# Kernel tuning notes

Measured on AMD Instinct MI355X. Metric: run time of the kernel, lower is better.

Reference implementation:

```python
import jax, jax.numpy as jnp
import numpy as np

NUM_HEADS = 8  # init num_heads


def setup_inputs() -> dict:
    key = jax.random.key(0)
    ks = jax.random.split(key, 8)
    B, N, C, G = 2, 256 * 256, 256, 512  # N hardcoded by original reshape(256*256)
    xq = jax.random.normal(ks[0], (B, N, C), jnp.float32)
    xk = jax.random.normal(ks[1], (B, N, C), jnp.float32)
    xv = jax.random.normal(ks[2], (B, N, C), jnp.float32)
    w_scale = C ** -0.5
    Wq = jax.random.normal(ks[3], (C, C), jnp.float32) * w_scale
    bq = jax.random.normal(ks[4], (C,), jnp.float32) * 0.02
    Wp = jax.random.normal(ks[5], (C, C), jnp.float32) * w_scale
    bp = jax.random.normal(ks[6], (C,), jnp.float32) * 0.02
    # Voronoi cell labels 1..G, each cell exactly N//G tokens, randomly scattered
    # over the 256x256 grid (irregular gather/scatter access, all cells < 1500 tokens).
    labels = jnp.repeat(jnp.arange(1, G + 1, dtype=jnp.int32), N // G)
    Voronoi = jnp.stack([
        jax.random.permutation(jax.random.fold_in(ks[7], b), labels) for b in range(B)
    ]).reshape(B, 256, 256)
    return {"xq": xq, "xk": xk, "xv": xv, "Wq": Wq, "bq": bq,
            "Wp": Wp, "bp": bp, "Voronoi": Voronoi, "num_groups": G}


def reference(xq, xk, xv, Wq, bq, Wp, bp, Voronoi, num_groups):
    B, N, C = xq.shape
    H = NUM_HEADS
    hd = C // H
    scale = hd ** -0.5  # qk_scale default: head_dim ** -0.5
    # NOTE: the original forward projects q, k AND v with self.q (shared weights/bias).
    # This (likely a bug upstream) is preserved faithfully here.
    q = (xq @ Wq.T + bq).reshape(B, N, H, hd)
    k = (xk @ Wq.T + bq).reshape(B, N, H, hd)
    v = (xv @ Wq.T + bq).reshape(B, N, H, hd)
    labels = Voronoi.reshape(B, N)
    order = jnp.argsort(labels, axis=1)   # [B, N] sort tokens by Voronoi cell id
    inv = jnp.argsort(order, axis=1)      # inverse permutation for scatter-back
    S = N // num_groups                   # tokens per cell (static)

    def gather(t):  # [B, N, H, hd] -> [B, G, S, H, hd] grouped by cell
        return jnp.take_along_axis(t, order[:, :, None, None], axis=1).reshape(B, num_groups, S, H, hd)

    qg = gather(q) * scale
    kg = gather(k)
    vg = gather(v)
    attn = jnp.einsum('bgshd,bgthd->bghst', qg, kg)   # per-cell scores [B,G,H,S,S]
    p = jax.nn.softmax(attn, axis=-1)                 # attn_drop=0 (eval)
    og = jnp.einsum('bghst,bgthd->bgshd', p, vg).reshape(B, N, H, hd)
    out = jnp.take_along_axis(og, inv[:, :, None, None], axis=1).reshape(B, N, C)
    return out @ Wp.T + bp                            # proj_drop=0 (eval)
```

## Files before the change

### kernel.cpp

```cpp
#include <hip/hip_runtime.h>
#include <hip/hip_bf16.h>

#define B_    2
#define NTOK  65536
#define C_    256
#define H_    8
#define HD_   32
#define G_    512
#define S_    128
#define BN    (B_*NTOK)
#define M3    (3*BN)

typedef __attribute__((ext_vector_type(8))) short short8;
typedef __attribute__((ext_vector_type(4))) float f32x4;

__device__ __forceinline__ ushort f2bf(float f) {
  __bf16 h = (__bf16)f;
  return __builtin_bit_cast(unsigned short, h);
}
__device__ __forceinline__ unsigned pk2(float lo, float hi) {
  return (unsigned)f2bf(lo) | ((unsigned)f2bf(hi) << 16);
}

__device__ __forceinline__ void gl16(const void* g, void* l) {
  __builtin_amdgcn_global_load_lds(
      (const __attribute__((address_space(1))) unsigned int*)g,
      (__attribute__((address_space(3))) unsigned int*)l, 16, 0, 0);
}

#define SW4(c, r) ((((c) ^ (r) ^ ((r) >> 2))) & 3)

__global__ __launch_bounds__(256) void k_prep(const float* __restrict__ Wq,
                                              const float* __restrict__ Wp,
                                              ushort* __restrict__ Wq_img,
                                              ushort* __restrict__ Wp_img) {
  int gid = blockIdx.x * 256 + threadIdx.x;
  int w = gid >> 13, rem = gid & 8191;
  int ks = rem >> 11, rem2 = rem & 2047;
  int r = rem2 >> 3, c = rem2 & 7;
  const float* W = w ? Wp : Wq;
  ushort* img = w ? Wp_img : Wq_img;
  const float4* s = reinterpret_cast<const float4*>(W + (size_t)r * 256 + ks * 64 + c * 8);
  float4 a = s[0], b = s[1];
  uint4 o;
  o.x = pk2(a.x, a.y); o.y = pk2(a.z, a.w);
  o.z = pk2(b.x, b.y); o.w = pk2(b.z, b.w);
  *reinterpret_cast<uint4*>(img + ks * 16384 + r * 64 + ((c ^ (r & 7)) << 3)) = o;
}

__global__ __launch_bounds__(256) void k_group(const int* __restrict__ vor,
                                               int* __restrict__ grp,
                                               int* __restrict__ cnt) {
  int idx = blockIdx.x * 256 + threadIdx.x;
  int b = idx >> 16;
  int n = idx & (NTOK - 1);
  int g = vor[idx] - 1;
  int pos = atomicAdd(&cnt[(b << 9) + g], 1);
  grp[((b << 9) + g) * S_ + pos] = n;
}

__global__ __launch_bounds__(512, 4) void k_proj_qkv(
    const float* __restrict__ xq, const float* __restrict__ xk,
    const float* __restrict__ xv, const ushort* __restrict__ Wq_img,
    const float* __restrict__ bq, ushort* __restrict__ qkv) {
  __shared__ ushort As[128 * 64];
  __shared__ ushort Bs[2][256 * 64];
  int mt = blockIdx.x;
  int t = mt >> 10;
  const float* A = (t == 0) ? xq : (t == 1) ? xk : xv;
  size_t abase = (size_t)(mt & 1023) * 128 * 256;
  int row0 = mt * 128;

  int tid = threadIdx.x, lane = tid & 63, wave = tid >> 6;
  int l15 = lane & 15, hi = lane >> 4;
  int wr = (wave >> 2) * 64, wc = (wave & 3) * 64;
  int sr = tid >> 2, sq = tid & 3;

  const float* aptr = A + abase + (size_t)sr * 256 + sq * 16;
  int boff = wave * 4096 + lane * 16;

  f32x4 acc[4][4] = {};
  float4 ar[2][4];
  {
    const float4* p = reinterpret_cast<const float4*>(aptr);
#pragma unroll
    for (int j = 0; j < 4; ++j) ar[0][j] = p[j];
  }
#pragma unroll
  for (int j = 0; j < 4; ++j)
    gl16((const char*)Wq_img + boff + j * 1024, (char*)Bs[0] + boff + j * 1024);

#pragma unroll
  for (int ks = 0; ks < 4; ++ks) {
    uint4 w0, w1;
    w0.x = pk2(ar[ks & 1][0].x, ar[ks & 1][0].y); w0.y = pk2(ar[ks & 1][0].z, ar[ks & 1][0].w);
    w0.z = pk2(ar[ks & 1][1].x, ar[ks & 1][1].y); w0.w = pk2(ar[ks & 1][1].z, ar[ks & 1][1].w);
    w1.x = pk2(ar[ks & 1][2].x, ar[ks & 1][2].y); w1.y = pk2(ar[ks & 1][2].z, ar[ks & 1][2].w);
    w1.z = pk2(ar[ks & 1][3].x, ar[ks & 1][3].y); w1.w = pk2(ar[ks & 1][3].z, ar[ks & 1][3].w);
    *reinterpret_cast<uint4*>(&As[sr * 64 + (((sq * 2) ^ (sr & 7)) << 3)]) = w0;
    *reinterpret_cast<uint4*>(&As[sr * 64 + (((sq * 2 + 1) ^ (sr & 7)) << 3)]) = w1;
    if (ks < 3) {
      const float4* p = reinterpret_cast<const float4*>(aptr + (ks + 1) * 64);
#pragma unroll
      for (int j = 0; j < 4; ++j) ar[(ks + 1) & 1][j] = p[j];
#pragma unroll
      for (int j = 0; j < 4; ++j)
        gl16((const char*)Wq_img + (ks + 1) * 32768 + boff + j * 1024,
             (char*)Bs[(ks + 1) & 1] + boff + j * 1024);
      asm volatile("s_waitcnt vmcnt(8)" ::: "memory");
    } else {
      asm volatile("s_waitcnt vmcnt(0)" ::: "memory");
    }
    asm volatile("s_waitcnt lgkmcnt(0)" ::: "memory");
    __builtin_amdgcn_s_barrier();
    const ushort* Bcur = Bs[ks & 1];
#pragma unroll
    for (int kk = 0; kk < 2; ++kk) {
      int ck = kk * 4 + hi;
      short8 af[4], bfr[4];
#pragma unroll
      for (int m = 0; m < 4; ++m) {
        int r = wr + m * 16 + l15;
        af[m] = *reinterpret_cast<const short8*>(&As[r * 64 + ((ck ^ (r & 7)) << 3)]);
      }
#pragma unroll
      for (int n = 0; n < 4; ++n) {
        int r = wc + n * 16 + l15;
        bfr[n] = *reinterpret_cast<const short8*>(&Bcur[r * 64 + ((ck ^ (r & 7)) << 3)]);
      }
#pragma unroll
      for (int m = 0; m < 4; ++m)
#pragma unroll
        for (int n = 0; n < 4; ++n)
          acc[m][n] = __builtin_amdgcn_mfma_f32_16x16x32_bf16(af[m], bfr[n], acc[m][n], 0, 0, 0);
    }
    asm volatile("s_waitcnt lgkmcnt(0)" ::: "memory");
    __builtin_amdgcn_s_barrier();
  }

  ushort* Ot = (ushort*)Bs;
#pragma unroll
  for (int n = 0; n < 4; ++n) {
    int col = wc + n * 16 + l15;
    float bv = bq[col];
    int c = col >> 3, ci = col & 7;
#pragma unroll
    for (int m = 0; m < 4; ++m) {
      int r0 = wr + m * 16 + hi * 4;
#pragma unroll
      for (int j = 0; j < 4; ++j) {
        int r = r0 + j;
        int slot = c ^ (((r >> 2) & 3) << 1);
        Ot[r * 256 + slot * 8 + ci] = f2bf(acc[m][n][j] + bv);
      }
    }
  }
  __syncthreads();
  {
    size_t gbase = (size_t)row0 * 256;
#pragma unroll
    for (int s = 0; s < 8; ++s) {
      int off = s * 4096 + tid * 8;
      int r = off >> 8, cc = (off >> 3) & 31;
      int slot = cc ^ (((r >> 2) & 3) << 1);
      *reinterpret_cast<uint4*>(qkv + gbase + off) =
          *reinterpret_cast<const uint4*>(Ot + r * 256 + slot * 8);
    }
  }
}

__global__ __launch_bounds__(256) void k_attn(const ushort* __restrict__ qkv,
                                              const int* __restrict__ grp,
                                              ushort* __restrict__ attn_out) {
  __shared__ int toks[128];
  __shared__ ushort PsB[128 * 128];
  __shared__ ushort Vt[32 * 128];
  ushort* Qs = PsB;
  ushort* Ks = PsB + 4096;
  ushort* Ps = PsB;

  int bid = blockIdx.x;
  int h = bid & 7, g = (bid >> 3) & (G_ - 1), b = bid >> 12;
  int tid = threadIdx.x, lane = tid & 63, wave = tid >> 6;
  int l15 = lane & 15, hi = lane >> 4;

  if (tid < 128) toks[tid] = grp[((b << 9) + g) * S_ + tid];
  __syncthreads();

  {
    int r = tid >> 1;
    int cp = (tid & 1) * 2;
    int tok = toks[r];
    size_t rowq = (size_t)(b * NTOK + tok) * 256 + h * 32;
    const uint4* q4 = reinterpret_cast<const uint4*>(qkv + rowq + cp * 8);
    const uint4* k4 = reinterpret_cast<const uint4*>(qkv + (size_t)BN * 256 + rowq + cp * 8);
    const uint4* v4 = reinterpret_cast<const uint4*>(qkv + (size_t)2 * BN * 256 + rowq + cp * 8);
    uint4 qa = q4[0], qb = q4[1];
    uint4 ka = k4[0], kb = k4[1];
    uint4 va = v4[0], vb = v4[1];
    *reinterpret_cast<uint4*>(&Qs[r * 32 + SW4(cp, r) * 8]) = qa;
    *reinterpret_cast<uint4*>(&Qs[r * 32 + SW4(cp + 1, r) * 8]) = qb;
    *reinterpret_cast<uint4*>(&Ks[r * 32 + SW4(cp, r) * 8]) = ka;
    *reinterpret_cast<uint4*>(&Ks[r * 32 + SW4(cp + 1, r) * 8]) = kb;
    int chunk_t = r >> 3, tl = r & 7;
    const ushort* pva = reinterpret_cast<const ushort*>(&va);
    const ushort* pvb = reinterpret_cast<const ushort*>(&vb);
#pragma unroll
    for (int e = 0; e < 8; ++e) {
      int ch = cp * 8 + e;
      Vt[ch * 128 + ((chunk_t ^ ((ch & 7) << 1)) << 3) + tl] = pva[e];
      int ch2 = ch + 8;
      Vt[ch2 * 128 + ((chunk_t ^ ((ch2 & 7) << 1)) << 3) + tl] = pvb[e];
    }
  }
  __syncthreads();

  f32x4 sacc[2][8] = {};
  {
    short8 aq[2], bk[8];
#pragma unroll
    for (int m = 0; m < 2; ++m) {
      int r = wave * 32 + m * 16 + l15;
      aq[m] = *reinterpret_cast<const short8*>(&Qs[r * 32 + SW4(hi, r) * 8]);
    }
#pragma unroll
    for (int n = 0; n < 8; ++n) {
      int r = n * 16 + l15;
      bk[n] = *reinterpret_cast<const short8*>(&Ks[r * 32 + SW4(hi, r) * 8]);
    }
#pragma unroll
    for (int m = 0; m < 2; ++m)
#pragma unroll
      for (int n = 0; n < 8; ++n)
        sacc[m][n] = __builtin_amdgcn_mfma_f32_16x16x32_bf16(aq[m], bk[n], sacc[m][n], 0, 0, 0);
  }
  __syncthreads();

  const float cexp = 0.17677669529663687f * 1.4426950408889634f;
#pragma unroll
  for (int m = 0; m < 2; ++m) {
#pragma unroll
    for (int j = 0; j < 4; ++j) {
      float mx = -1e30f;
#pragma unroll
      for (int n = 0; n < 8; ++n) mx = fmaxf(mx, sacc[m][n][j]);
#pragma unroll
      for (int d = 1; d < 16; d <<= 1) mx = fmaxf(mx, __shfl_xor(mx, d));
      float pv[8], sum = 0.f;
#pragma unroll
      for (int n = 0; n < 8; ++n) { pv[n] = exp2f((sacc[m][n][j] - mx) * cexp); sum += pv[n]; }
#pragma unroll
      for (int d = 1; d < 16; d <<= 1) sum += __shfl_xor(sum, d);
      float inv = 1.0f / sum;
      int row = wave * 32 + m * 16 + hi * 4 + j;
#pragma unroll
      for (int n = 0; n < 8; ++n) {
        int col = n * 16 + l15;
        int chunk = col >> 3;
        Ps[row * 128 + ((chunk ^ (row & 7)) << 3) + (col & 7)] = f2bf(pv[n] * inv);
      }
    }
  }
  __syncthreads();

  f32x4 oacc[2][2] = {};
#pragma unroll
  for (int kk = 0; kk < 4; ++kk) {
    int k0 = kk * 32 + hi * 8;
    int chunk = k0 >> 3;
    short8 pa[2], bv[2];
#pragma unroll
    for (int m = 0; m < 2; ++m) {
      int r = wave * 32 + m * 16 + l15;
      pa[m] = *reinterpret_cast<const short8*>(&Ps[r * 128 + ((chunk ^ (r & 7)) << 3)]);
    }
#pragma unroll
    for (int n = 0; n < 2; ++n) {
      int ch = n * 16 + l15;
      bv[n] = *reinterpret_cast<const short8*>(&Vt[ch * 128 + ((chunk ^ ((ch & 7) << 1)) << 3)]);
    }
#pragma unroll
    for (int m = 0; m < 2; ++m)
#pragma unroll
      for (int n = 0; n < 2; ++n)
        oacc[m][n] = __builtin_amdgcn_mfma_f32_16x16x32_bf16(pa[m], bv[n], oacc[m][n], 0, 0, 0);
  }

  __syncthreads();
  ushort* Ot = Ps;
#pragma unroll
  for (int m = 0; m < 2; ++m) {
    int rb = wave * 32 + m * 16 + hi * 4;
#pragma unroll
    for (int j = 0; j < 4; ++j)
#pragma unroll
      for (int n = 0; n < 2; ++n)
        Ot[(rb + j) * 32 + n * 16 + l15] = f2bf(oacc[m][n][j]);
  }
  __syncthreads();
  {
    int tr = tid >> 1, part = tid & 1;
    int tok = toks[tr];
    size_t base = ((size_t)(b * NTOK + tok)) * 256 + h * 32 + part * 16;
    const uint4* src = reinterpret_cast<const uint4*>(Ot + tr * 32 + part * 16);
    uint4 v0 = src[0], v1 = src[1];
    *reinterpret_cast<uint4*>(attn_out + base) = v0;
    *reinterpret_cast<uint4*>(attn_out + base + 8) = v1;
  }
}

__global__ __launch_bounds__(512, 4) void k_proj_out(
    const ushort* __restrict__ Abf, const ushort* __restrict__ Wp_img,
    const float* __restrict__ bp, float* __restrict__ out) {
  __shared__ ushort As[128 * 64];
  __shared__ ushort Bs[2][256 * 64];
  int mt = blockIdx.x;
  int row0 = mt * 128;

  int tid = threadIdx.x, lane = tid & 63, wave = tid >> 6;
  int l15 = lane & 15, hi = lane >> 4;
  int wr = (wave >> 2) * 64, wc = (wave & 3) * 64;
  int sr = tid >> 2, sq = tid & 3;

  const ushort* aptr = Abf + (size_t)(row0 + sr) * 256 + sq * 16;
  int boff = wave * 4096 + lane * 16;

  f32x4 acc[4][4] = {};
  uint4 ar[2][2];
  {
    const uint4* p = reinterpret_cast<const uint4*>(aptr);
    ar[0][0] = p[0]; ar[0][1] = p[1];
  }
#pragma unroll
  for (int j = 0; j < 4; ++j)
    gl16((const char*)Wp_img + boff + j * 1024, (char*)Bs[0] + boff + j * 1024);

#pragma unroll
  for (int ks = 0; ks < 4; ++ks) {
    *reinterpret_cast<uint4*>(&As[sr * 64 + (((sq * 2) ^ (sr & 7)) << 3)]) = ar[ks & 1][0];
    *reinterpret_cast<uint4*>(&As[sr * 64 + (((sq * 2 + 1) ^ (sr & 7)) << 3)]) = ar[ks & 1][1];
    if (ks < 3) {
      const uint4* p = reinterpret_cast<const uint4*>(aptr + (ks + 1) * 64);
      ar[(ks + 1) & 1][0] = p[0]; ar[(ks + 1) & 1][1] = p[1];
#pragma unroll
      for (int j = 0; j < 4; ++j)
        gl16((const char*)Wp_img + (ks + 1) * 32768 + boff + j * 1024,
             (char*)Bs[(ks + 1) & 1] + boff + j * 1024);
      asm volatile("s_waitcnt vmcnt(6)" ::: "memory");
    } else {
      asm volatile("s_waitcnt vmcnt(0)" ::: "memory");
    }
    asm volatile("s_waitcnt lgkmcnt(0)" ::: "memory");
    __builtin_amdgcn_s_barrier();
    const ushort* Bcur = Bs[ks & 1];
#pragma unroll
    for (int kk = 0; kk < 2; ++kk) {
      int ck = kk * 4 + hi;
      short8 af[4], bfr[4];
#pragma unroll
      for (int m = 0; m < 4; ++m) {
        int r = wr + m * 16 + l15;
        af[m] = *reinterpret_cast<const short8*>(&As[r * 64 + ((ck ^ (r & 7)) << 3)]);
      }
#pragma unroll
      for (int n = 0; n < 4; ++n) {
        int r = wc + n * 16 + l15;
        bfr[n] = *reinterpret_cast<const short8*>(&Bcur[r * 64 + ((ck ^ (r & 7)) << 3)]);
      }
#pragma unroll
      for (int m = 0; m < 4; ++m)
#pragma unroll
        for (int n = 0; n < 4; ++n)
          acc[m][n] = __builtin_amdgcn_mfma_f32_16x16x32_bf16(af[m], bfr[n], acc[m][n], 0, 0, 0);
    }
    asm volatile("s_waitcnt lgkmcnt(0)" ::: "memory");
    __builtin_amdgcn_s_barrier();
  }

  float* Of = (float*)Bs;
#pragma unroll
  for (int hf = 0; hf < 2; ++hf) {
    if (hf) __syncthreads();
    if ((wave >> 2) == hf) {
#pragma unroll
      for (int n = 0; n < 4; ++n) {
        int col = wc + n * 16 + l15;
        float bv = bp[col];
        int c = col >> 2, ci = col & 3;
#pragma unroll
        for (int m = 0; m < 4; ++m) {
          int lr = m * 16 + hi * 4;
#pragma unroll
          for (int j = 0; j < 4; ++j) {
            int r = lr + j;
            int slot = c ^ (((r >> 2) & 3) << 2);
            Of[r * 256 + slot * 4 + ci] = acc[m][n][j] + bv;
          }
        }
      }
    }
    __syncthreads();
    size_t gbase = (size_t)(row0 + hf * 64) * 256;
#pragma unroll
    for (int s = 0; s < 8; ++s) {
      int off = s * 2048 + tid * 4;
      int r = off >> 8, cc = (off >> 2) & 63;
      int slot = cc ^ (((r >> 2) & 3) << 2);
      *reinterpret_cast<float4*>(out + gbase + off) =
          *reinterpret_cast<const float4*>(Of + r * 256 + slot * 4);
    }
  }
}

extern "C" void kernel_launch(void* const* d_in, const int* in_sizes, int n_in,
                              void* d_out, int out_size, void* d_ws, size_t ws_size,
                              hipStream_t stream) {
  const float* xq = (const float*)d_in[0];
  const float* xk = (const float*)d_in[1];
  const float* xv = (const float*)d_in[2];
  const float* Wq = (const float*)d_in[3];
  const float* bq = (const float*)d_in[4];
  const float* Wp = (const float*)d_in[5];
  const float* bp = (const float*)d_in[6];
  const int*   vor = (const int*)d_in[7];

  char* ws = (char*)d_ws;
  ushort* qkv    = (ushort*)ws;
  ushort* attn   = (ushort*)(ws + (size_t)201326592);
  int*    grp    = (int*)(ws + (size_t)268435456);
  int*    cnt    = (int*)(ws + (size_t)268959744);
  ushort* Wq_img = (ushort*)(ws + (size_t)268963840);
  ushort* Wp_img = (ushort*)(ws + (size_t)269094912);

  hipMemsetAsync(cnt, 0, B_ * G_ * sizeof(int), stream);
  k_prep<<<dim3(64), dim3(256), 0, stream>>>(Wq, Wp, Wq_img, Wp_img);
  k_group<<<dim3(BN / 256), dim3(256), 0, stream>>>(vor, grp, cnt);
  k_proj_qkv<<<dim3(M3 / 128), dim3(512), 0, stream>>>(xq, xk, xv, Wq_img, bq, qkv);
  k_attn<<<dim3(B_ * G_ * H_), dim3(256), 0, stream>>>(qkv, grp, attn);
  k_proj_out<<<dim3(BN / 128), dim3(512), 0, stream>>>(attn, Wp_img, bp, (float*)d_out);
}
```

Measured before the change: 318.1 us.

## Split QKV projection into 128x128 tiles with K=32 double-buffered pipeline

The QKV projection kernel now uses 256-thread blocks that each compute a 128x128 output tile, so twice as many blocks are launched. The K loop runs in 8 steps of 32 instead of 4 steps of 64. Both the A and the weight tiles are double-buffered, so the next step's global loads overlap the current MFMA step. The weight image layout and its swizzle are rebuilt to match the K=32 tiling. The aim is more blocks and more overlap per CU, at the cost of reading and converting the fp32 activations twice (once per column half) and running more barriers.

Measured after the change: 342.4 us. +7.6%, slower.

```diff
diff --git a/kernel.cpp b/kernel.cpp
--- a/kernel.cpp
+++ b/kernel.cpp
@@ -29,6 +29,7 @@
 }
 
 #define SW4(c, r) ((((c) ^ (r) ^ ((r) >> 2))) & 3)
+#define SWK32(c, r) ((((c) ^ ((r) >> 1))) & 3)
 
 __global__ __launch_bounds__(256) void k_prep(const float* __restrict__ Wq,
                                               const float* __restrict__ Wp,
@@ -36,16 +37,24 @@
                                               ushort* __restrict__ Wp_img) {
   int gid = blockIdx.x * 256 + threadIdx.x;
   int w = gid >> 13, rem = gid & 8191;
-  int ks = rem >> 11, rem2 = rem & 2047;
-  int r = rem2 >> 3, c = rem2 & 7;
-  const float* W = w ? Wp : Wq;
-  ushort* img = w ? Wp_img : Wq_img;
-  const float4* s = reinterpret_cast<const float4*>(W + (size_t)r * 256 + ks * 64 + c * 8);
-  float4 a = s[0], b = s[1];
-  uint4 o;
-  o.x = pk2(a.x, a.y); o.y = pk2(a.z, a.w);
-  o.z = pk2(b.x, b.y); o.w = pk2(b.z, b.w);
-  *reinterpret_cast<uint4*>(img + ks * 16384 + r * 64 + ((c ^ (r & 7)) << 3)) = o;
+  if (w == 0) {
+    int ks = rem >> 10, r = (rem >> 2) & 255, c = rem & 3;
+    const float4* s = reinterpret_cast<const float4*>(Wq + (size_t)r * 256 + ks * 32 + c * 8);
+    float4 a = s[0], b = s[1];
+    uint4 o;
+    o.x = pk2(a.x, a.y); o.y = pk2(a.z, a.w);
+    o.z = pk2(b.x, b.y); o.w = pk2(b.z, b.w);
+    *reinterpret_cast<uint4*>(Wq_img + ks * 8192 + r * 32 + (SWK32(c, r) << 3)) = o;
+  } else {
+    int ks = rem >> 11, rem2 = rem & 2047;
+    int r = rem2 >> 3, c = rem2 & 7;
+    const float4* s = reinterpret_cast<const float4*>(Wp + (size_t)r * 256 + ks * 64 + c * 8);
+    float4 a = s[0], b = s[1];
+    uint4 o;
+    o.x = pk2(a.x, a.y); o.y = pk2(a.z, a.w);
+    o.z = pk2(b.x, b.y); o.w = pk2(b.z, b.w);
+    *reinterpret_cast<uint4*>(Wp_img + ks * 16384 + r * 64 + ((c ^ (r & 7)) << 3)) = o;
+  }
 }
 
 __global__ __launch_bounds__(256) void k_group(const int* __restrict__ vor,
@@ -59,112 +68,133 @@
   grp[((b << 9) + g) * S_ + pos] = n;
 }
 
-__global__ __launch_bounds__(512, 4) void k_proj_qkv(
+__global__ __launch_bounds__(256, 4) void k_proj_qkv(
     const float* __restrict__ xq, const float* __restrict__ xk,
     const float* __restrict__ xv, const ushort* __restrict__ Wq_img,
     const float* __restrict__ bq, ushort* __restrict__ qkv) {
-  __shared__ ushort As[128 * 64];
-  __shared__ ushort Bs[2][256 * 64];
-  int mt = blockIdx.x;
+  __shared__ ushort lds[24576];
+  ushort* AsB[2] = { lds, lds + 4096 };
+  ushort* BsB[2] = { lds + 8192, lds + 16384 };
+  BsB[0] = lds + 8192; BsB[1] = lds + 12288;
+
+  int bid = blockIdx.x;
+  int mt = bid >> 1, nt = bid & 1;
   int t = mt >> 10;
   const float* A = (t == 0) ? xq : (t == 1) ? xk : xv;
   size_t abase = (size_t)(mt & 1023) * 128 * 256;
-  int row0 = mt * 128;
+  int row0 = mt * 128, col0 = nt * 128;
 
   int tid = threadIdx.x, lane = tid & 63, wave = tid >> 6;
   int l15 = lane & 15, hi = lane >> 4;
-  int wr = (wave >> 2) * 64, wc = (wave & 3) * 64;
-  int sr = tid >> 2, sq = tid & 3;
-
-  const float* aptr = A + abase + (size_t)sr * 256 + sq * 16;
-  int boff = wave * 4096 + lane * 16;
+  int wr = (wave >> 1) * 64, wc = (wave & 1) * 64;
+  int sr = tid >> 1, sc2 = (tid & 1) * 2;
+
+  const float* aptr = A + abase + (size_t)sr * 256 + sc2 * 8;
+  const char* bimg = (const char*)Wq_img + nt * 8192;
+  int boff = wave * 2048 + lane * 16;
 
   f32x4 acc[4][4] = {};
-  float4 ar[2][4];
+  float4 a[2][4];
+
   {
     const float4* p = reinterpret_cast<const float4*>(aptr);
 #pragma unroll
-    for (int j = 0; j < 4; ++j) ar[0][j] = p[j];
-  }
-#pragma unroll
-  for (int j = 0; j < 4; ++j)
-    gl16((const char*)Wq_img + boff + j * 1024, (char*)Bs[0] + boff + j * 1024);
-
-#pragma unroll
-  for (int ks = 0; ks < 4; ++ks) {
+    for (int j = 0; j < 4; ++j) a[0][j] = p[j];
+  }
+  gl16(bimg + boff, (char*)BsB[0] + boff);
+  gl16(bimg + boff + 1024, (char*)BsB[0] + boff + 1024);
+  {
+    const float4* p = reinterpret_cast<const float4*>(aptr + 32);
+#pragma unroll
+    for (int j = 0; j < 4; ++j) a[1][j] = p[j];
+  }
+  {
     uint4 w0, w1;
-    w0.x = pk2(ar[ks & 1][0].x, ar[ks & 1][0].y); w0.y = pk2(ar[ks & 1][0].z, ar[ks & 1][0].w);
-    w0.z = pk2(ar[ks & 1][1].x, ar[ks & 1][1].y); w0.w = pk2(ar[ks & 1][1].z, ar[ks & 1][1].w);
-    w1.x = pk2(ar[ks & 1][2].x, ar[ks & 1][2].y); w1.y = pk2(ar[ks & 1][2].z, ar[ks & 1][2].w);
-    w1.z = pk2(ar[ks & 1][3].x, ar[ks & 1][3].y); w1.w = pk2(ar[ks & 1][3].z, ar[ks & 1][3].w);
-    *reinterpret_cast<uint4*>(&As[sr * 64 + (((sq * 2) ^ (sr & 7)) << 3)]) = w0;
-    *reinterpret_cast<uint4*>(&As[sr * 64 + (((sq * 2 + 1) ^ (sr & 7)) << 3)]) = w1;
-    if (ks < 3) {
-      const float4* p = reinterpret_cast<const float4*>(aptr + (ks + 1) * 64);
-#pragma unroll
-      for (int j = 0; j < 4; ++j) ar[(ks + 1) & 1][j] = p[j];
-#pragma unroll
-      for (int j = 0; j < 4; ++j)
-        gl16((const char*)Wq_img + (ks + 1) * 32768 + boff + j * 1024,
-             (char*)Bs[(ks + 1) & 1] + boff + j * 1024);
-      asm volatile("s_waitcnt vmcnt(8)" ::: "memory");
+    w0.x = pk2(a[0][0].x, a[0][0].y); w0.y = pk2(a[0][0].z, a[0][0].w);
+    w0.z = pk2(a[0][1].x, a[0][1].y); w0.w = pk2(a[0][1].z, a[0][1].w);
+    w1.x = pk2(a[0][2].x, a[0][2].y); w1.y = pk2(a[0][2].z, a[0][2].w);
+    w1.z = pk2(a[0][3].x, a[0][3].y); w1.w = pk2(a[0][3].z, a[0][3].w);
+    *reinterpret_cast<uint4*>(&AsB[0][sr * 32 + (SWK32(sc2, sr) << 3)]) = w0;
+    *reinterpret_cast<uint4*>(&AsB[0][sr * 32 + (SWK32(sc2 + 1, sr) << 3)]) = w1;
+  }
+  asm volatile("s_waitcnt vmcnt(4)" ::: "memory");
+  asm volatile("s_waitcnt lgkmcnt(0)" ::: "memory");
+  __builtin_amdgcn_s_barrier();
+
+#pragma unroll
+  for (int ks = 0; ks < 8; ++ks) {
+    const int cur = ks & 1, alt = cur ^ 1;
+    if (ks < 7) {
+      gl16(bimg + (ks + 1) * 16384 + boff, (char*)BsB[alt] + boff);
+      gl16(bimg + (ks + 1) * 16384 + boff + 1024, (char*)BsB[alt] + boff + 1024);
+      uint4 w0, w1;
+      w0.x = pk2(a[alt][0].x, a[alt][0].y); w0.y = pk2(a[alt][0].z, a[alt][0].w);
+      w0.z = pk2(a[alt][1].x, a[alt][1].y); w0.w = pk2(a[alt][1].z, a[alt][1].w);
+      w1.x = pk2(a[alt][2].x, a[alt][2].y); w1.y = pk2(a[alt][2].z, a[alt][2].w);
+      w1.z = pk2(a[alt][3].x, a[alt][3].y); w1.w = pk2(a[alt][3].z, a[alt][3].w);
+      *reinterpret_cast<uint4*>(&AsB[alt][sr * 32 + (SWK32(sc2, sr) << 3)]) = w0;
+      *reinterpret_cast<uint4*>(&AsB[alt][sr * 32 + (SWK32(sc2 + 1, sr) << 3)]) = w1;
+    }
+    if (ks < 6) {
+      const float4* p = reinterpret_cast<const float4*>(aptr + (ks + 2) * 32);
+#pragma unroll
+      for (int j = 0; j < 4; ++j) a[cur][j] = p[j];
+    }
+    {
+      const ushort* Ac = AsB[cur];
+      const ushort* Bc = BsB[cur];
+      short8 af[4], bf[4];
+#pragma unroll
+      for (int m = 0; m < 4; ++m) {
+        int r = wr + m * 16 + l15;
+        af[m] = *reinterpret_cast<const short8*>(&Ac[r * 32 + (SWK32(hi, r) << 3)]);
+      }
+#pragma unroll
+      for (int n = 0; n < 4; ++n) {
+        int r = wc + n * 16 + l15;
+        bf[n] = *reinterpret_cast<const short8*>(&Bc[r * 32 + (SWK32(hi, r) << 3)]);
+      }
+#pragma unroll
+      for (int m = 0; m < 4; ++m)
+#pragma unroll
+        for (int n = 0; n < 4; ++n)
+          acc[m][n] = __builtin_amdgcn_mfma_f32_16x16x32_bf16(af[m], bf[n], acc[m][n], 0, 0, 0);
+    }
+    if (ks < 6) {
+      asm volatile("s_waitcnt vmcnt(4)" ::: "memory");
     } else {
       asm volatile("s_waitcnt vmcnt(0)" ::: "memory");
     }
     asm volatile("s_waitcnt lgkmcnt(0)" ::: "memory");
     __builtin_amdgcn_s_barrier();
-    const ushort* Bcur = Bs[ks & 1];
-#pragma unroll
-    for (int kk = 0; kk < 2; ++kk) {
-      int ck = kk * 4 + hi;
-      short8 af[4], bfr[4];
-#pragma unroll
-      for (int m = 0; m < 4; ++m) {
-        int r = wr + m * 16 + l15;
-        af[m] = *reinterpret_cast<const short8*>(&As[r * 64 + ((ck ^ (r & 7)) << 3)]);
-      }
-#pragma unroll
-      for (int n = 0; n < 4; ++n) {
-        int r = wc + n * 16 + l15;
-        bfr[n] = *reinterpret_cast<const short8*>(&Bcur[r * 64 + ((ck ^ (r & 7)) << 3)]);
-      }
-#pragma unroll
-      for (int m = 0; m < 4; ++m)
-#pragma unroll
-        for (int n = 0; n < 4; ++n)
-          acc[m][n] = __builtin_amdgcn_mfma_f32_16x16x32_bf16(af[m], bfr[n], acc[m][n], 0, 0, 0);
-    }
-    asm volatile("s_waitcnt lgkmcnt(0)" ::: "memory");
-    __builtin_amdgcn_s_barrier();
-  }
-
-  ushort* Ot = (ushort*)Bs;
+  }
+
+  ushort* Ot = lds;
 #pragma unroll
   for (int n = 0; n < 4; ++n) {
-    int col = wc + n * 16 + l15;
-    float bv = bq[col];
-    int c = col >> 3, ci = col & 7;
+    int lc = wc + n * 16 + l15;
+    float bv = bq[col0 + lc];
+    int c = lc >> 3, ci = lc & 7;
 #pragma unroll
     for (int m = 0; m < 4; ++m) {
       int r0 = wr + m * 16 + hi * 4;
 #pragma unroll
       for (int j = 0; j < 4; ++j) {
         int r = r0 + j;
-        int slot = c ^ (((r >> 2) & 3) << 1);
-        Ot[r * 256 + slot * 8 + ci] = f2bf(acc[m][n][j] + bv);
-      }
-    }
-  }
-  __syncthreads();
-  {
-    size_t gbase = (size_t)row0 * 256;
+        int slot = (c ^ ((r >> 2) & 3)) & 15;
+        Ot[r * 128 + slot * 8 + ci] = f2bf(acc[m][n][j] + bv);
+      }
+    }
+  }
+  __syncthreads();
+  {
 #pragma unroll
     for (int s = 0; s < 8; ++s) {
-      int off = s * 4096 + tid * 8;
-      int r = off >> 8, cc = (off >> 3) & 31;
-      int slot = cc ^ (((r >> 2) & 3) << 1);
-      *reinterpret_cast<uint4*>(qkv + gbase + off) =
-          *reinterpret_cast<const uint4*>(Ot + r * 256 + slot * 8);
+      int i = s * 2048 + tid * 8;
+      int r = i >> 7, c = (tid & 15);
+      int slot = (c ^ ((r >> 2) & 3)) & 15;
+      *reinterpret_cast<uint4*>(qkv + (size_t)(row0 + r) * 256 + col0 + c * 8) =
+          *reinterpret_cast<const uint4*>(Ot + r * 128 + slot * 8);
     }
   }
 }
@@ -435,7 +465,7 @@
   hipMemsetAsync(cnt, 0, B_ * G_ * sizeof(int), stream);
   k_prep<<<dim3(64), dim3(256), 0, stream>>>(Wq, Wp, Wq_img, Wp_img);
   k_group<<<dim3(BN / 256), dim3(256), 0, stream>>>(vor, grp, cnt);
-  k_proj_qkv<<<dim3(M3 / 128), dim3(512), 0, stream>>>(xq, xk, xv, Wq_img, bq, qkv);
+  k_proj_qkv<<<dim3((M3 / 128) * 2), dim3(256), 0, stream>>>(xq, xk, xv, Wq_img, bq, qkv);
   k_attn<<<dim3(B_ * G_ * H_), dim3(256), 0, stream>>>(qkv, grp, attn);
   k_proj_out<<<dim3(BN / 128), dim3(512), 0, stream>>>(attn, Wp_img, bp, (float*)d_out);
 }
```

## Fuse attention and output projection into one per-cell kernel

Applied to the files above, without the earlier changes.

Merges the per-(cell,head) attention kernel and the output projection GEMM into a single kernel in which each block handles one Voronoi cell and loops over all 8 heads. Each head's output is accumulated straight into the projection result through a per-head Wp slice staged in LDS, and the final fp32 result is scattered to token rows. This removes the bf16 attention intermediate write/read and one kernel launch. In exchange there are far fewer blocks (1024 instead of 8192), a serial head loop with many barriers, larger LDS use per block, and scattered row writes to the output.

After: 341.7 us. 1.07x slower.

```diff
diff --git a/kernel.cpp b/kernel.cpp
--- a/kernel.cpp
+++ b/kernel.cpp
@@ -29,6 +29,7 @@
 }
 
 #define SW4(c, r) ((((c) ^ (r) ^ ((r) >> 2))) & 3)
+#define SWK32(c, r) ((((c) ^ ((r) >> 1))) & 3)
 
 __global__ __launch_bounds__(256) void k_prep(const float* __restrict__ Wq,
                                               const float* __restrict__ Wp,
@@ -36,16 +37,24 @@
                                               ushort* __restrict__ Wp_img) {
   int gid = blockIdx.x * 256 + threadIdx.x;
   int w = gid >> 13, rem = gid & 8191;
-  int ks = rem >> 11, rem2 = rem & 2047;
-  int r = rem2 >> 3, c = rem2 & 7;
-  const float* W = w ? Wp : Wq;
-  ushort* img = w ? Wp_img : Wq_img;
-  const float4* s = reinterpret_cast<const float4*>(W + (size_t)r * 256 + ks * 64 + c * 8);
-  float4 a = s[0], b = s[1];
-  uint4 o;
-  o.x = pk2(a.x, a.y); o.y = pk2(a.z, a.w);
-  o.z = pk2(b.x, b.y); o.w = pk2(b.z, b.w);
-  *reinterpret_cast<uint4*>(img + ks * 16384 + r * 64 + ((c ^ (r & 7)) << 3)) = o;
+  if (w == 0) {
+    int ks = rem >> 11, rem2 = rem & 2047;
+    int r = rem2 >> 3, c = rem2 & 7;
+    const float4* s = reinterpret_cast<const float4*>(Wq + (size_t)r * 256 + ks * 64 + c * 8);
+    float4 a = s[0], b = s[1];
+    uint4 o;
+    o.x = pk2(a.x, a.y); o.y = pk2(a.z, a.w);
+    o.z = pk2(b.x, b.y); o.w = pk2(b.z, b.w);
+    *reinterpret_cast<uint4*>(Wq_img + ks * 16384 + r * 64 + ((c ^ (r & 7)) << 3)) = o;
+  } else {
+    int h = rem >> 10, r = (rem >> 2) & 255, c = rem & 3;
+    const float4* s = reinterpret_cast<const float4*>(Wp + (size_t)r * 256 + h * 32 + c * 8);
+    float4 a = s[0], b = s[1];
+    uint4 o;
+    o.x = pk2(a.x, a.y); o.y = pk2(a.z, a.w);
+    o.z = pk2(b.x, b.y); o.w = pk2(b.z, b.w);
+    *reinterpret_cast<uint4*>(Wp_img + h * 8192 + r * 32 + (SWK32(c, r) << 3)) = o;
+  }
 }
 
 __global__ __launch_bounds__(256) void k_group(const int* __restrict__ vor,
@@ -169,90 +178,90 @@
   }
 }
 
-__global__ __launch_bounds__(256) void k_attn(const ushort* __restrict__ qkv,
-                                              const int* __restrict__ grp,
-                                              ushort* __restrict__ attn_out) {
+__global__ __launch_bounds__(512) void k_attn_proj(
+    const ushort* __restrict__ qkv, const int* __restrict__ grp,
+    const ushort* __restrict__ Wp_img, const float* __restrict__ bp,
+    float* __restrict__ out) {
   __shared__ int toks[128];
   __shared__ ushort PsB[128 * 128];
   __shared__ ushort Vt[32 * 128];
+  __shared__ ushort Oh[128 * 32];
+  __shared__ ushort WpS[256 * 32];
   ushort* Qs = PsB;
   ushort* Ks = PsB + 4096;
   ushort* Ps = PsB;
 
   int bid = blockIdx.x;
-  int h = bid & 7, g = (bid >> 3) & (G_ - 1), b = bid >> 12;
+  int g = bid & (G_ - 1), b = bid >> 9;
   int tid = threadIdx.x, lane = tid & 63, wave = tid >> 6;
   int l15 = lane & 15, hi = lane >> 4;
+  int strip = wave * 16;
+  int mg = wave >> 1, ng = wave & 1;
 
   if (tid < 128) toks[tid] = grp[((b << 9) + g) * S_ + tid];
   __syncthreads();
 
-  {
-    int r = tid >> 1;
-    int cp = (tid & 1) * 2;
-    int tok = toks[r];
-    size_t rowq = (size_t)(b * NTOK + tok) * 256 + h * 32;
-    const uint4* q4 = reinterpret_cast<const uint4*>(qkv + rowq + cp * 8);
-    const uint4* k4 = reinterpret_cast<const uint4*>(qkv + (size_t)BN * 256 + rowq + cp * 8);
-    const uint4* v4 = reinterpret_cast<const uint4*>(qkv + (size_t)2 * BN * 256 + rowq + cp * 8);
-    uint4 qa = q4[0], qb = q4[1];
-    uint4 ka = k4[0], kb = k4[1];
-    uint4 va = v4[0], vb = v4[1];
-    *reinterpret_cast<uint4*>(&Qs[r * 32 + SW4(cp, r) * 8]) = qa;
-    *reinterpret_cast<uint4*>(&Qs[r * 32 + SW4(cp + 1, r) * 8]) = qb;
-    *reinterpret_cast<uint4*>(&Ks[r * 32 + SW4(cp, r) * 8]) = ka;
-    *reinterpret_cast<uint4*>(&Ks[r * 32 + SW4(cp + 1, r) * 8]) = kb;
-    int chunk_t = r >> 3, tl = r & 7;
-    const ushort* pva = reinterpret_cast<const ushort*>(&va);
-    const ushort* pvb = reinterpret_cast<const ushort*>(&vb);
-#pragma unroll
-    for (int e = 0; e < 8; ++e) {
-      int ch = cp * 8 + e;
-      Vt[ch * 128 + ((chunk_t ^ ((ch & 7) << 1)) << 3) + tl] = pva[e];
-      int ch2 = ch + 8;
-      Vt[ch2 * 128 + ((chunk_t ^ ((ch2 & 7) << 1)) << 3) + tl] = pvb[e];
-    }
-  }
-  __syncthreads();
-
-  f32x4 sacc[2][8] = {};
-  {
-    short8 aq[2], bk[8];
-#pragma unroll
-    for (int m = 0; m < 2; ++m) {
-      int r = wave * 32 + m * 16 + l15;
-      aq[m] = *reinterpret_cast<const short8*>(&Qs[r * 32 + SW4(hi, r) * 8]);
-    }
-#pragma unroll
-    for (int n = 0; n < 8; ++n) {
-      int r = n * 16 + l15;
-      bk[n] = *reinterpret_cast<const short8*>(&Ks[r * 32 + SW4(hi, r) * 8]);
-    }
-#pragma unroll
-    for (int m = 0; m < 2; ++m)
+  int wpoff = wave * 1024 + lane * 16;
+  gl16((const char*)Wp_img + wpoff, (char*)WpS + wpoff);
+  gl16((const char*)Wp_img + 8192 + wpoff, (char*)WpS + wpoff + 8192);
+
+  f32x4 acc[2][8] = {};
+
+  int r_st = tid >> 2, cp = tid & 3;
+  int tok_st = toks[r_st];
+  size_t rowq = (size_t)(b * NTOK + tok_st) * 256;
+
+  for (int h = 0; h < 8; ++h) {
+    {
+      size_t base = rowq + h * 32 + cp * 8;
+      uint4 qa = *reinterpret_cast<const uint4*>(qkv + base);
+      uint4 ka = *reinterpret_cast<const uint4*>(qkv + (size_t)BN * 256 + base);
+      uint4 va = *reinterpret_cast<const uint4*>(qkv + (size_t)2 * BN * 256 + base);
+      *reinterpret_cast<uint4*>(&Qs[r_st * 32 + SW4(cp, r_st) * 8]) = qa;
+      *reinterpret_cast<uint4*>(&Ks[r_st * 32 + SW4(cp, r_st) * 8]) = ka;
+      int chunk_t = r_st >> 3, tl = r_st & 7;
+      const ushort* pv_ = reinterpret_cast<const ushort*>(&va);
+#pragma unroll
+      for (int e = 0; e < 8; ++e) {
+        int ch = cp * 8 + e;
+        Vt[ch * 128 + ((chunk_t ^ ((ch & 7) << 1)) << 3) + tl] = pv_[e];
+      }
+    }
+    asm volatile("s_waitcnt lgkmcnt(0)" ::: "memory");
+    __builtin_amdgcn_s_barrier();
+
+    f32x4 sacc[8] = {};
+    {
+      int ra = strip + l15;
+      short8 aq = *reinterpret_cast<const short8*>(&Qs[ra * 32 + SW4(hi, ra) * 8]);
+      short8 bk[8];
+#pragma unroll
+      for (int n = 0; n < 8; ++n) {
+        int r = n * 16 + l15;
+        bk[n] = *reinterpret_cast<const short8*>(&Ks[r * 32 + SW4(hi, r) * 8]);
+      }
 #pragma unroll
       for (int n = 0; n < 8; ++n)
-        sacc[m][n] = __builtin_amdgcn_mfma_f32_16x16x32_bf16(aq[m], bk[n], sacc[m][n], 0, 0, 0);
-  }
-  __syncthreads();
-
-  const float cexp = 0.17677669529663687f * 1.4426950408889634f;
-#pragma unroll
-  for (int m = 0; m < 2; ++m) {
+        sacc[n] = __builtin_amdgcn_mfma_f32_16x16x32_bf16(aq, bk[n], sacc[n], 0, 0, 0);
+    }
+    asm volatile("s_waitcnt lgkmcnt(0)" ::: "memory");
+    __builtin_amdgcn_s_barrier();
+
+    const float cexp = 0.17677669529663687f * 1.4426950408889634f;
 #pragma unroll
     for (int j = 0; j < 4; ++j) {
       float mx = -1e30f;
 #pragma unroll
-      for (int n = 0; n < 8; ++n) mx = fmaxf(mx, sacc[m][n][j]);
+      for (int n = 0; n < 8; ++n) mx = fmaxf(mx, sacc[n][j]);
 #pragma unroll
       for (int d = 1; d < 16; d <<= 1) mx = fmaxf(mx, __shfl_xor(mx, d));
       float pv[8], sum = 0.f;
 #pragma unroll
-      for (int n = 0; n < 8; ++n) { pv[n] = exp2f((sacc[m][n][j] - mx) * cexp); sum += pv[n]; }
+      for (int n = 0; n < 8; ++n) { pv[n] = exp2f((sacc[n][j] - mx) * cexp); sum += pv[n]; }
 #pragma unroll
       for (int d = 1; d < 16; d <<= 1) sum += __shfl_xor(sum, d);
       float inv = 1.0f / sum;
-      int row = wave * 32 + m * 16 + hi * 4 + j;
+      int row = strip + hi * 4 + j;
 #pragma unroll
       for (int n = 0; n < 8; ++n) {
         int col = n * 16 + l15;
@@ -260,154 +269,94 @@
         Ps[row * 128 + ((chunk ^ (row & 7)) << 3) + (col & 7)] = f2bf(pv[n] * inv);
       }
     }
-  }
-  __syncthreads();
-
-  f32x4 oacc[2][2] = {};
-#pragma unroll
-  for (int kk = 0; kk < 4; ++kk) {
-    int k0 = kk * 32 + hi * 8;
-    int chunk = k0 >> 3;
-    short8 pa[2], bv[2];
-#pragma unroll
-    for (int m = 0; m < 2; ++m) {
-      int r = wave * 32 + m * 16 + l15;
-      pa[m] = *reinterpret_cast<const short8*>(&Ps[r * 128 + ((chunk ^ (r & 7)) << 3)]);
+    asm volatile("s_waitcnt lgkmcnt(0)" ::: "memory");
+    __builtin_amdgcn_s_barrier();
+
+    f32x4 oacc[2] = {};
+#pragma unroll
+    for (int kk = 0; kk < 4; ++kk) {
+      int chunk = kk * 4 + hi;
+      int rp = strip + l15;
+      short8 pa = *reinterpret_cast<const short8*>(&Ps[rp * 128 + ((chunk ^ (rp & 7)) << 3)]);
+      short8 bv[2];
+#pragma unroll
+      for (int n = 0; n < 2; ++n) {
+        int ch = n * 16 + l15;
+        bv[n] = *reinterpret_cast<const short8*>(&Vt[ch * 128 + ((chunk ^ ((ch & 7) << 1)) << 3)]);
+      }
+#pragma unroll
+      for (int n = 0; n < 2; ++n)
+        oacc[n] = __builtin_amdgcn_mfma_f32_16x16x32_bf16(pa, bv[n], oacc[n], 0, 0, 0);
     }
 #pragma unroll
     for (int n = 0; n < 2; ++n) {
-      int ch = n * 16 + l15;
-      bv[n] = *reinterpret_cast<const short8*>(&Vt[ch * 128 + ((chunk ^ ((ch & 7) << 1)) << 3)]);
-    }
-#pragma unroll
-    for (int m = 0; m < 2; ++m)
-#pragma unroll
-      for (int n = 0; n < 2; ++n)
-        oacc[m][n] = __builtin_amdgcn_mfma_f32_16x16x32_bf16(pa[m], bv[n], oacc[m][n], 0, 0, 0);
-  }
-
-  __syncthreads();
-  ushort* Ot = Ps;
-#pragma unroll
-  for (int m = 0; m < 2; ++m) {
-    int rb = wave * 32 + m * 16 + hi * 4;
-#pragma unroll
-    for (int j = 0; j < 4; ++j)
-#pragma unroll
-      for (int n = 0; n < 2; ++n)
-        Ot[(rb + j) * 32 + n * 16 + l15] = f2bf(oacc[m][n][j]);
-  }
-  __syncthreads();
-  {
-    int tr = tid >> 1, part = tid & 1;
-    int tok = toks[tr];
-    size_t base = ((size_t)(b * NTOK + tok)) * 256 + h * 32 + part * 16;
-    const uint4* src = reinterpret_cast<const uint4*>(Ot + tr * 32 + part * 16);
-    uint4 v0 = src[0], v1 = src[1];
-    *reinterpret_cast<uint4*>(attn_out + base) = v0;
-    *reinterpret_cast<uint4*>(attn_out + base + 8) = v1;
-  }
-}
-
-__global__ __launch_bounds__(512, 4) void k_proj_out(
-    const ushort* __restrict__ Abf, const ushort* __restrict__ Wp_img,
-    const float* __restrict__ bp, float* __restrict__ out) {
-  __shared__ ushort As[128 * 64];
-  __shared__ ushort Bs[2][256 * 64];
-  int mt = blockIdx.x;
-  int row0 = mt * 128;
-
-  int tid = threadIdx.x, lane = tid & 63, wave = tid >> 6;
-  int l15 = lane & 15, hi = lane >> 4;
-  int wr = (wave >> 2) * 64, wc = (wave & 3) * 64;
-  int sr = tid >> 2, sq = tid & 3;
-
-  const ushort* aptr = Abf + (size_t)(row0 + sr) * 256 + sq * 16;
-  int boff = wave * 4096 + lane * 16;
-
-  f32x4 acc[4][4] = {};
-  uint4 ar[2][2];
-  {
-    const uint4* p = reinterpret_cast<const uint4*>(aptr);
-    ar[0][0] = p[0]; ar[0][1] = p[1];
-  }
-#pragma unroll
-  for (int j = 0; j < 4; ++j)
-    gl16((const char*)Wp_img + boff + j * 1024, (char*)Bs[0] + boff + j * 1024);
-
-#pragma unroll
-  for (int ks = 0; ks < 4; ++ks) {
-    *reinterpret_cast<uint4*>(&As[sr * 64 + (((sq * 2) ^ (sr & 7)) << 3)]) = ar[ks & 1][0];
-    *reinterpret_cast<uint4*>(&As[sr * 64 + (((sq * 2 + 1) ^ (sr & 7)) << 3)]) = ar[ks & 1][1];
-    if (ks < 3) {
-      const uint4* p = reinterpret_cast<const uint4*>(aptr + (ks + 1) * 64);
-      ar[(ks + 1) & 1][0] = p[0]; ar[(ks + 1) & 1][1] = p[1];
-#pragma unroll
-      for (int j = 0; j < 4; ++j)
-        gl16((const char*)Wp_img + (ks + 1) * 32768 + boff + j * 1024,
-             (char*)Bs[(ks + 1) & 1] + boff + j * 1024);
-      asm volatile("s_waitcnt vmcnt(6)" ::: "memory");
-    } else {
-      asm volatile("s_waitcnt vmcnt(0)" ::: "memory");
-    }
-    asm volatile("s_waitcnt lgkmcnt(0)" ::: "memory");
-    __builtin_amdgcn_s_barrier();
-    const ushort* Bcur = Bs[ks & 1];
-#pragma unroll
-    for (int kk = 0; kk < 2; ++kk) {
-      int ck = kk * 4 + hi;
-      short8 af[4], bfr[4];
-#pragma unroll
-      for (int m = 0; m < 4; ++m) {
-        int r = wr + m * 16 + l15;
-        af[m] = *reinterpret_cast<const short8*>(&As[r * 64 + ((ck ^ (r & 7)) << 3)]);
-      }
-#pragma unroll
-      for (int n = 0; n < 4; ++n) {
-        int r = wc + n * 16 + l15;
-        bfr[n] = *reinterpret_cast<const short8*>(&Bcur[r * 64 + ((ck ^ (r & 7)) << 3)]);
-      }
-#pragma unroll
-      for (int m = 0; m < 4; ++m)
-#pragma unroll
-        for (int n = 0; n < 4; ++n)
-          acc[m][n] = __builtin_amdgcn_mfma_f32_16x16x32_bf16(af[m], bfr[n], acc[m][n], 0, 0, 0);
-    }
-    asm volatile("s_waitcnt lgkmcnt(0)" ::: "memory");
-    __builtin_amdgcn_s_barrier();
-  }
-
-  float* Of = (float*)Bs;
-#pragma unroll
-  for (int hf = 0; hf < 2; ++hf) {
-    if (hf) __syncthreads();
-    if ((wave >> 2) == hf) {
-#pragma unroll
-      for (int n = 0; n < 4; ++n) {
-        int col = wc + n * 16 + l15;
+#pragma unroll
+      for (int j = 0; j < 4; ++j) {
+        int row = strip + hi * 4 + j;
+        int col = n * 16 + l15;
+        Oh[row * 32 + (SWK32(col >> 3, row) << 3) + (col & 7)] = f2bf(oacc[n][j]);
+      }
+    }
+    asm volatile("s_waitcnt vmcnt(0)" ::: "memory");
+    asm volatile("s_waitcnt lgkmcnt(0)" ::: "memory");
+    __builtin_amdgcn_s_barrier();
+
+    {
+      short8 af[2], bf[8];
+#pragma unroll
+      for (int m = 0; m < 2; ++m) {
+        int r = mg * 32 + m * 16 + l15;
+        af[m] = *reinterpret_cast<const short8*>(&Oh[r * 32 + (SWK32(hi, r) << 3)]);
+      }
+#pragma unroll
+      for (int n = 0; n < 8; ++n) {
+        int r = ng * 128 + n * 16 + l15;
+        bf[n] = *reinterpret_cast<const short8*>(&WpS[r * 32 + (SWK32(hi, r) << 3)]);
+      }
+#pragma unroll
+      for (int m = 0; m < 2; ++m)
+#pragma unroll
+        for (int n = 0; n < 8; ++n)
+          acc[m][n] = __builtin_amdgcn_mfma_f32_16x16x32_bf16(af[m], bf[n], acc[m][n], 0, 0, 0);
+    }
+    asm volatile("s_waitcnt lgkmcnt(0)" ::: "memory");
+    __builtin_amdgcn_s_barrier();
+    if (h < 7) {
+      gl16((const char*)Wp_img + (h + 1) * 16384 + wpoff, (char*)WpS + wpoff);
+      gl16((const char*)Wp_img + (h + 1) * 16384 + 8192 + wpoff, (char*)WpS + wpoff + 8192);
+    }
+  }
+
+  float* Of = (float*)PsB;
+#pragma unroll
+  for (int q = 0; q < 4; ++q) {
+    __syncthreads();
+    if (mg == q) {
+#pragma unroll
+      for (int n = 0; n < 8; ++n) {
+        int col = ng * 128 + n * 16 + l15;
         float bv = bp[col];
         int c = col >> 2, ci = col & 3;
 #pragma unroll
-        for (int m = 0; m < 4; ++m) {
-          int lr = m * 16 + hi * 4;
+        for (int m = 0; m < 2; ++m) {
 #pragma unroll
           for (int j = 0; j < 4; ++j) {
-            int r = lr + j;
-            int slot = c ^ (((r >> 2) & 3) << 2);
-            Of[r * 256 + slot * 4 + ci] = acc[m][n][j] + bv;
+            int lr = m * 16 + hi * 4 + j;
+            int slot = c ^ (((lr >> 2) & 3) << 2);
+            Of[lr * 256 + slot * 4 + ci] = acc[m][n][j] + bv;
           }
         }
       }
     }
     __syncthreads();
-    size_t gbase = (size_t)(row0 + hf * 64) * 256;
-#pragma unroll
-    for (int s = 0; s < 8; ++s) {
+#pragma unroll
+    for (int s = 0; s < 4; ++s) {
       int off = s * 2048 + tid * 4;
-      int r = off >> 8, cc = (off >> 2) & 63;
-      int slot = cc ^ (((r >> 2) & 3) << 2);
-      *reinterpret_cast<float4*>(out + gbase + off) =
-          *reinterpret_cast<const float4*>(Of + r * 256 + slot * 4);
+      int lr = off >> 8, cc = (off >> 2) & 63;
+      int slot = cc ^ (((lr >> 2) & 3) << 2);
+      int tok = toks[q * 32 + lr];
+      *reinterpret_cast<float4*>(out + ((size_t)(b * NTOK + tok)) * 256 + cc * 4) =
+          *reinterpret_cast<const float4*>(Of + lr * 256 + slot * 4);
     }
   }
 }
@@ -426,16 +375,14 @@
 
   char* ws = (char*)d_ws;
   ushort* qkv    = (ushort*)ws;
-  ushort* attn   = (ushort*)(ws + (size_t)201326592);
-  int*    grp    = (int*)(ws + (size_t)268435456);
-  int*    cnt    = (int*)(ws + (size_t)268959744);
-  ushort* Wq_img = (ushort*)(ws + (size_t)268963840);
-  ushort* Wp_img = (ushort*)(ws + (size_t)269094912);
+  int*    grp    = (int*)(ws + (size_t)201326592);
+  int*    cnt    = (int*)(ws + (size_t)201850880);
+  ushort* Wq_img = (ushort*)(ws + (size_t)201854976);
+  ushort* Wp_img = (ushort*)(ws + (size_t)201986048);
 
   hipMemsetAsync(cnt, 0, B_ * G_ * sizeof(int), stream);
   k_prep<<<dim3(64), dim3(256), 0, stream>>>(Wq, Wp, Wq_img, Wp_img);
   k_group<<<dim3(BN / 256), dim3(256), 0, stream>>>(vor, grp, cnt);
   k_proj_qkv<<<dim3(M3 / 128), dim3(512), 0, stream>>>(xq, xk, xv, Wq_img, bq, qkv);
-  k_attn<<<dim3(B_ * G_ * H_), dim3(256), 0, stream>>>(qkv, grp, attn);
-  k_proj_out<<<dim3(BN / 128), dim3(512), 0, stream>>>(attn, Wp_img, bp, (float*)d_out);
-}
+  k_attn_proj<<<dim3(B_ * G_), dim3(512), 0, stream>>>(qkv, grp, Wp_img, bp, (float*)d_out);
+}
```
